# Performance work log

Hardware: AMD Instinct MI355X
Metric: run time of the kernel (lower is better)

## Reference

```python
import jax, jax.numpy as jnp
import numpy as np
import math

B, S, D, H = 2, 2048, 1024, 16
HD = D // H  # head_dim = 64


def setup_inputs() -> dict:
    key = jax.random.key(0)
    k1, k2, k3, k4, k5 = jax.random.split(key, 5)
    scale_in = 1.0 / math.sqrt(D)
    return {
        "x": jax.random.normal(k1, (B, S, D), dtype=jnp.float32),
        "Wqkv": jax.random.normal(k2, (3 * D, D), dtype=jnp.float32) * scale_in,
        "bqkv": jax.random.normal(k3, (3 * D,), dtype=jnp.float32) * 0.01,
        "Wout": jax.random.normal(k4, (D, D), dtype=jnp.float32) * scale_in,
        "bout": jax.random.normal(k5, (D,), dtype=jnp.float32) * 0.01,
    }


def reference(x, Wqkv, bqkv, Wout, bout):
    Bs, Sl, Dm = x.shape
    # qkv projection: torch Linear is x @ W.T + b
    qkv = x @ Wqkv.T + bqkv                        # [B,S,3D]
    qkv = qkv.reshape(Bs, Sl, 3, H, HD)
    q, k, v = qkv[:, :, 0], qkv[:, :, 1], qkv[:, :, 2]  # each [B,S,H,d]
    softmax_scale = 1.0 / math.sqrt(HD)
    # NOTE: source einsum 'bshd,btjd->bsht' sums k over its head axis j.
    # Equivalent efficient form: pre-sum k (and v) over heads.
    k_sum = k.sum(axis=2)                          # [B,S,d]
    v_sum = v.sum(axis=2)                          # [B,S,d]
    scores = jnp.einsum('bshd,btd->bsht', q, k_sum) * softmax_scale  # [B,S,H,T]
    causal_mask = jnp.triu(jnp.ones((Sl, Sl), dtype=bool), k=1)      # [S,T]
    scores = jnp.where(causal_mask[None, :, None, :], -jnp.inf, scores)
    attn = jax.nn.softmax(scores, axis=-1)
    # dropout p=0.0 / eval mode -> identity
    out = jnp.einsum('bsht,btd->bshd', attn, v_sum)  # [B,S,H,d]
    out = out.reshape(Bs, Sl, Dm)
    return out @ Wout.T + bout
```

## Files before the change

### kernel.cpp

```cpp
#include <hip/hip_runtime.h>


#define S_LEN 2048
#define DIM 1024

using floatx4 = __attribute__((ext_vector_type(4))) float;
using halfx8  = __attribute__((ext_vector_type(8))) _Float16;
using halfx4  = __attribute__((ext_vector_type(4))) _Float16;
using halfx2  = __attribute__((ext_vector_type(2))) _Float16;
using fp16x2  = __attribute__((ext_vector_type(2))) __fp16;

__device__ __forceinline__ floatx4 mfma16(halfx8 a, halfx8 b, floatx4 c) {
  return __builtin_amdgcn_mfma_f32_16x16x32_f16(a, b, c, 0, 0, 0);
}

__device__ __forceinline__ void gll16(const void* g, void* l) {
  __builtin_amdgcn_global_load_lds(
      (const __attribute__((address_space(1))) void*)g,
      (__attribute__((address_space(3))) void*)l, 16, 0, 0);
}

__global__ __launch_bounds__(256) void prep_all(
    const float* __restrict__ x, const float* __restrict__ wqkv,
    const float* __restrict__ bqkv, const float* __restrict__ wout,
    _Float16* __restrict__ xb, _Float16* __restrict__ wcomb,
    _Float16* __restrict__ woutb, float* __restrict__ bcomb) {
  int bx = blockIdx.x;
  if (bx < 6144) {
    size_t i4 = ((size_t)bx * 256 + threadIdx.x) * 4;
    const float* src;
    _Float16* dst;
    size_t off;
    if (i4 < 4194304) { src = x; dst = xb; off = i4; }
    else if (i4 < 5242880) { src = wqkv; dst = wcomb; off = i4 - 4194304; }
    else { src = wout; dst = woutb; off = i4 - 5242880; }
    float4 v = *(const float4*)(src + off);
    halfx4 o;
    o[0] = (_Float16)v.x; o[1] = (_Float16)v.y;
    o[2] = (_Float16)v.z; o[3] = (_Float16)v.w;
    *(halfx4*)(dst + off) = o;
  } else {
    int gid = (bx - 6144) * 256 + threadIdx.x;
    int c = gid >> 10, j = gid & 1023;
    int row0 = (c < 64) ? (1024 + c) : (2048 + c - 64);
    float s = 0.f;
#pragma unroll
    for (int h = 0; h < 16; ++h) s += wqkv[(size_t)(row0 + h * 64) * 1024 + j];
    wcomb[(size_t)1024 * 1024 + gid] = (_Float16)s;
    if (gid < 1024) bcomb[gid] = bqkv[gid];
    if (gid < 128) {
      int b0 = (gid < 64) ? (1024 + gid) : (2048 + gid - 64);
      float sb = 0.f;
#pragma unroll
      for (int h = 0; h < 16; ++h) sb += bqkv[b0 + h * 64];
      bcomb[1024 + gid] = sb;
    }
  }
}

template <int MODE>
__global__ __launch_bounds__(256, 6) void gemm_t5(
    const _Float16* __restrict__ A, const _Float16* __restrict__ W,
    const float* __restrict__ bias, void* __restrict__ Cv,
    _Float16* __restrict__ kbo, _Float16* __restrict__ vto) {
  const int K = 1024;
  __shared__ _Float16 As[64][64];
  __shared__ _Float16 Ws[64][64];
  int tid = threadIdx.x;
  int lane = tid & 63, w = tid >> 6, ln = lane & 15, q4 = lane >> 4;
  int m0 = blockIdx.x * 64, n0 = blockIdx.y * 64;
  int rr = lane >> 3, gg = ((lane & 7) ^ rr) * 8;
  const _Float16* agp = A + (size_t)(m0 + w * 16 + rr) * K + gg;
  const _Float16* wgp = W + (size_t)(n0 + w * 16 + rr) * K + gg;
  floatx4 acc[4] = {};
  for (int kt = 0; kt < K; kt += 64) {
    __syncthreads();
    gll16(agp + kt, &As[w * 16][0]);
    gll16(agp + (size_t)8 * K + kt, &As[w * 16 + 8][0]);
    gll16(wgp + kt, &Ws[w * 16][0]);
    gll16(wgp + (size_t)8 * K + kt, &Ws[w * 16 + 8][0]);
    __syncthreads();
#pragma unroll
    for (int kh = 0; kh < 2; ++kh) {
      int sw = ((q4 + 4 * kh) ^ (ln & 7)) * 8;
      halfx8 bf = *(const halfx8*)&Ws[w * 16 + ln][sw];
#pragma unroll
      for (int mf = 0; mf < 4; ++mf) {
        halfx8 af = *(const halfx8*)&As[mf * 16 + ln][sw];
        acc[mf] = mfma16(af, bf, acc[mf]);
      }
    }
  }
  const float qscale = 0.18033688011112042f;
  int col = n0 + w * 16 + ln;
  float bv = bias[col];
  if constexpr (MODE == 1) {
#pragma unroll
    for (int mf = 0; mf < 4; ++mf)
#pragma unroll
      for (int i = 0; i < 4; ++i) {
        int row = m0 + mf * 16 + q4 * 4 + i;
        ((float*)Cv)[(size_t)row * 1024 + col] = acc[mf][i] + bv;
      }
  } else {
    if (col < 1024) {
#pragma unroll
      for (int mf = 0; mf < 4; ++mf)
#pragma unroll
        for (int i = 0; i < 4; ++i) {
          int row = m0 + mf * 16 + q4 * 4 + i;
          ((_Float16*)Cv)[(size_t)row * 1024 + col] =
              (_Float16)((acc[mf][i] + bv) * qscale);
        }
    } else if (col < 1088) {
      int ck = col - 1024;
#pragma unroll
      for (int mf = 0; mf < 4; ++mf)
#pragma unroll
        for (int i = 0; i < 4; ++i) {
          int row = m0 + mf * 16 + q4 * 4 + i;
          kbo[(size_t)row * 64 + ck] = (_Float16)(acc[mf][i] + bv);
        }
    } else {
      int d = col - 1088;
#pragma unroll
      for (int mf = 0; mf < 4; ++mf) {
        int row0 = m0 + mf * 16 + q4 * 4;
        int bb = row0 >> 11, sps = row0 & 2047;
        int blk = sps & ~127, tl = sps & 127;
        int p0 = (tl >> 6) * 64 + ((tl >> 2) & 3) * 8 + ((tl >> 4) & 3) * 2;
        _Float16* basep = &vto[((size_t)((bb << 6) + d)) * S_LEN + blk];
        halfx2 lo, hi;
        lo[0] = (_Float16)(acc[mf][0] + bv);
        lo[1] = (_Float16)(acc[mf][1] + bv);
        hi[0] = (_Float16)(acc[mf][2] + bv);
        hi[1] = (_Float16)(acc[mf][3] + bv);
        *(halfx2*)&basep[p0] = lo;
        *(halfx2*)&basep[p0 + 32] = hi;
      }
    }
  }
}

__global__ __launch_bounds__(512, 4) void flash_attn14(
    const _Float16* __restrict__ Qb, const _Float16* __restrict__ kb,
    const _Float16* __restrict__ vtb, _Float16* __restrict__ aob) {
  __shared__ _Float16 Ks[2][128][64];
  __shared__ _Float16 Vt[2][64][128];
  int tid = threadIdx.x;
  int lane = tid & 63, w = tid >> 6, ln = lane & 15, q4 = lane >> 4;
  int bx = (int)blockIdx.x;
  int lo = bx & 255;
  int b = lo & 1;
  int crow = (bx >> 8) ? (255 - (lo >> 1)) : (lo >> 1);
  int s0 = crow * 8;
  int s = s0 + w;
  size_t bS = (size_t)b * S_LEN;

  int rr = lane >> 3, ggk = ((lane & 7) ^ rr) * 8;
  const _Float16* kgp = kb + (bS + w * 16 + rr) * 64 + ggk;
  int vr = lane >> 4;
  int vhalf = (lane >> 3) & 1, vg = lane & 7;
  const _Float16* vgp[2];
#pragma unroll
  for (int j = 0; j < 2; ++j) {
    int row = w * 8 + 4 * j + vr;
    vgp[j] = vtb + ((size_t)b * 64 + row) * S_LEN + vhalf * 64 +
             ((vg ^ (row & 7)) * 8);
  }
  int swk0 = (q4 ^ (ln & 7)) * 8;
  int swk1 = ((q4 + 4) ^ (ln & 7)) * 8;

  const _Float16* qp = Qb + (bS + s) * DIM + ln * 64 + q4 * 8;
  halfx8 bq0 = *(const halfx8*)qp, bq1 = *(const halfx8*)(qp + 32);

  float m_run = -1e30f, l_run = 0.f;
  floatx4 oacc[4] = {};
  int nt = (crow >> 4) + 1;

  gll16(kgp, &Ks[0][w * 16][0]);
  gll16(kgp + (size_t)8 * 64, &Ks[0][w * 16 + 8][0]);
  gll16(vgp[0], &Vt[0][w * 8][0]);
  gll16(vgp[1], &Vt[0][w * 8 + 4][0]);
  __syncthreads();

  for (int it = 0; it < nt; ++it) {
    int cur = it & 1, nxt = cur ^ 1;
    if (it + 1 < nt) {
      int t1 = (it + 1) << 7;
      gll16(kgp + (size_t)t1 * 64, &Ks[nxt][w * 16][0]);
      gll16(kgp + (size_t)(t1 + 8) * 64, &Ks[nxt][w * 16 + 8][0]);
      gll16(vgp[0] + t1, &Vt[nxt][w * 8][0]);
      gll16(vgp[1] + t1, &Vt[nxt][w * 8 + 4][0]);
    }
    int t0 = it << 7;

    floatx4 sf[2][4];
    __builtin_amdgcn_s_setprio(1);
#pragma unroll
    for (int tq = 0; tq < 2; ++tq)
#pragma unroll
      for (int tf = 0; tf < 4; ++tf) {
        halfx8 ak0 = *(const halfx8*)&Ks[cur][tq * 64 + tf * 16 + ln][swk0];
        halfx8 ak1 = *(const halfx8*)&Ks[cur][tq * 64 + tf * 16 + ln][swk1];
        floatx4 z = {};
        z = mfma16(ak0, bq0, z);
        sf[tq][tf] = mfma16(ak1, bq1, z);
      }
    __builtin_amdgcn_s_setprio(0);
    if (it == nt - 1) {
#pragma unroll
      for (int tq = 0; tq < 2; ++tq)
#pragma unroll
        for (int tf = 0; tf < 4; ++tf)
#pragma unroll
          for (int i = 0; i < 4; ++i) {
            int t = t0 + tq * 64 + tf * 16 + q4 * 4 + i;
            if (t > s) sf[tq][tf][i] = -1e30f;
          }
    }
    float tm = -1e30f;
#pragma unroll
    for (int tq = 0; tq < 2; ++tq)
#pragma unroll
      for (int tf = 0; tf < 4; ++tf)
        tm = fmaxf(tm, fmaxf(fmaxf(sf[tq][tf][0], sf[tq][tf][1]),
                             fmaxf(sf[tq][tf][2], sf[tq][tf][3])));
    tm = fmaxf(tm, __shfl_xor(tm, 16));
    tm = fmaxf(tm, __shfl_xor(tm, 32));
    if (!__all(tm <= m_run + 8.f)) {
      float mn = fmaxf(m_run, tm);
      float alpha = exp2f(m_run - mn);
      m_run = mn;
      l_run *= alpha;
#pragma unroll
      for (int n2 = 0; n2 < 4; ++n2)
#pragma unroll
        for (int i = 0; i < 4; ++i) oacc[n2][i] *= alpha;
    }
    float rs = 0.f;
    unsigned bpw[4][4];
#pragma unroll
    for (int tq = 0; tq < 2; ++tq)
#pragma unroll
      for (int tf = 0; tf < 4; ++tf) {
        float p0 = exp2f(sf[tq][tf][0] - m_run);
        float p1 = exp2f(sf[tq][tf][1] - m_run);
        float p2 = exp2f(sf[tq][tf][2] - m_run);
        float p3 = exp2f(sf[tq][tf][3] - m_run);
        rs += (p0 + p1) + (p2 + p3);
        union { fp16x2 h; unsigned u; } c0, c1;
        c0.h = __builtin_amdgcn_cvt_pkrtz(p0, p1);
        c1.h = __builtin_amdgcn_cvt_pkrtz(p2, p3);
        bpw[2 * tq][tf] = c0.u;
        bpw[2 * tq + 1][tf] = c1.u;
      }
    rs += __shfl_xor(rs, 16);
    rs += __shfl_xor(rs, 32);
    l_run += rs;
    __builtin_amdgcn_s_setprio(1);
#pragma unroll
    for (int kc = 0; kc < 4; ++kc) {
      union { unsigned u[4]; halfx8 v; } bpu;
#pragma unroll
      for (int ww = 0; ww < 4; ++ww) bpu.u[ww] = bpw[kc][ww];
      int half = (kc >> 1) * 64;
      int sw = ((q4 + 4 * (kc & 1)) ^ (ln & 7)) * 8;
#pragma unroll
      for (int n2 = 0; n2 < 4; ++n2) {
        halfx8 av = *(const halfx8*)&Vt[cur][n2 * 16 + ln][half + sw];
        oacc[n2] = mfma16(av, bpu.v, oacc[n2]);
      }
    }
    __builtin_amdgcn_s_setprio(0);
    __syncthreads();
  }
  float inv = 1.0f / l_run;
#pragma unroll
  for (int n2 = 0; n2 < 4; ++n2) {
    halfx4 o;
#pragma unroll
    for (int i = 0; i < 4; ++i) o[i] = (_Float16)(oacc[n2][i] * inv);
    *(halfx4*)(aob + (bS + s) * DIM + ln * 64 + n2 * 16 + q4 * 4) = o;
  }
}

extern "C" void kernel_launch(void* const* d_in, const int* in_sizes, int n_in,
                              void* d_out, int out_size, void* d_ws,
                              size_t ws_size, hipStream_t stream) {
  const float* x    = (const float*)d_in[0];
  const float* wqkv = (const float*)d_in[1];
  const float* bqkv = (const float*)d_in[2];
  const float* wout = (const float*)d_in[3];
  const float* bout = (const float*)d_in[4];
  float* out = (float*)d_out;
  char* ws = (char*)d_ws;
  _Float16* xb    = (_Float16*)(ws);
  _Float16* qb    = (_Float16*)(ws + (8u << 20));
  _Float16* aob   = (_Float16*)(ws + (16u << 20));
  _Float16* kb    = (_Float16*)(ws + (24u << 20));
  _Float16* vtb   = (_Float16*)(ws + (24u << 20) + (512u << 10));
  _Float16* wcomb = (_Float16*)(ws + (25u << 20));
  _Float16* woutb = (_Float16*)(ws + (27u << 20) + (512u << 10));
  float*    bcomb = (float*)(ws + (29u << 20) + (512u << 10));

  hipLaunchKernelGGL(prep_all, dim3(6656), dim3(256), 0, stream,
                     x, wqkv, bqkv, wout, xb, wcomb, woutb, bcomb);
  hipLaunchKernelGGL((gemm_t5<0>), dim3(64, 18), dim3(256), 0, stream,
                     xb, wcomb, bcomb, (void*)qb, kb, vtb);
  hipLaunchKernelGGL(flash_attn14, dim3(512), dim3(512), 0, stream,
                     qb, kb, vtb, aob);
  hipLaunchKernelGGL((gemm_t5<1>), dim3(64, 16), dim3(256), 0, stream,
                     aob, woutb, bout, (void*)out, nullptr, nullptr);
}
```

Baseline: 157.9 us.

## Shrink attention blocks to 4 waves and drop K/V LDS double buffering

Each attention block now has 4 waves covering 4 query rows instead of 8 waves covering 8, and the grid doubles to 1024 blocks, with the causal load-balancing pairing extended to four row groups. K/V tiles are single-buffered in LDS, with a sync before and after each synchronous load in place of prefetching the next tile. This halves LDS per block, allowing more resident blocks and a finer work split. In exchange each wave issues more loads per tile, load latency is no longer overlapped with compute, and total K/V traffic rises because fewer rows share each tile.

```diff
diff --git a/kernel.cpp b/kernel.cpp
--- a/kernel.cpp
+++ b/kernel.cpp
@@ -142,29 +142,30 @@
   }
 }
 
-__global__ __launch_bounds__(512, 4) void flash_attn14(
+__global__ __launch_bounds__(256, 4) void flash_attn15(
     const _Float16* __restrict__ Qb, const _Float16* __restrict__ kb,
     const _Float16* __restrict__ vtb, _Float16* __restrict__ aob) {
-  __shared__ _Float16 Ks[2][128][64];
-  __shared__ _Float16 Vt[2][64][128];
+  __shared__ _Float16 Ks[128][64];
+  __shared__ _Float16 Vt[64][128];
   int tid = threadIdx.x;
   int lane = tid & 63, w = tid >> 6, ln = lane & 15, q4 = lane >> 4;
   int bx = (int)blockIdx.x;
-  int lo = bx & 255;
-  int b = lo & 1;
-  int crow = (bx >> 8) ? (255 - (lo >> 1)) : (lo >> 1);
-  int s0 = crow * 8;
+  int q = bx >> 8, lo = bx & 255;
+  int b = lo & 1, p = lo >> 1;
+  int crow = (q == 0) ? p : (q == 1) ? (255 - p) : (q == 2) ? (256 + p)
+                                                            : (511 - p);
+  int s0 = crow * 4;
   int s = s0 + w;
   size_t bS = (size_t)b * S_LEN;
 
   int rr = lane >> 3, ggk = ((lane & 7) ^ rr) * 8;
-  const _Float16* kgp = kb + (bS + w * 16 + rr) * 64 + ggk;
+  const _Float16* kgp = kb + (bS + w * 32 + rr) * 64 + ggk;
   int vr = lane >> 4;
   int vhalf = (lane >> 3) & 1, vg = lane & 7;
-  const _Float16* vgp[2];
-#pragma unroll
-  for (int j = 0; j < 2; ++j) {
-    int row = w * 8 + 4 * j + vr;
+  const _Float16* vgp[4];
+#pragma unroll
+  for (int j = 0; j < 4; ++j) {
+    int row = w * 16 + 4 * j + vr;
     vgp[j] = vtb + ((size_t)b * 64 + row) * S_LEN + vhalf * 64 +
              ((vg ^ (row & 7)) * 8);
   }
@@ -176,24 +177,18 @@
 
   float m_run = -1e30f, l_run = 0.f;
   floatx4 oacc[4] = {};
-  int nt = (crow >> 4) + 1;
-
-  gll16(kgp, &Ks[0][w * 16][0]);
-  gll16(kgp + (size_t)8 * 64, &Ks[0][w * 16 + 8][0]);
-  gll16(vgp[0], &Vt[0][w * 8][0]);
-  gll16(vgp[1], &Vt[0][w * 8 + 4][0]);
-  __syncthreads();
+  int nt = (crow >> 5) + 1;
 
   for (int it = 0; it < nt; ++it) {
-    int cur = it & 1, nxt = cur ^ 1;
-    if (it + 1 < nt) {
-      int t1 = (it + 1) << 7;
-      gll16(kgp + (size_t)t1 * 64, &Ks[nxt][w * 16][0]);
-      gll16(kgp + (size_t)(t1 + 8) * 64, &Ks[nxt][w * 16 + 8][0]);
-      gll16(vgp[0] + t1, &Vt[nxt][w * 8][0]);
-      gll16(vgp[1] + t1, &Vt[nxt][w * 8 + 4][0]);
-    }
     int t0 = it << 7;
+    __syncthreads();
+#pragma unroll
+    for (int j = 0; j < 4; ++j)
+      gll16(kgp + (size_t)(t0 + 8 * j) * 64, &Ks[w * 32 + 8 * j][0]);
+#pragma unroll
+    for (int j = 0; j < 4; ++j)
+      gll16(vgp[j] + t0, &Vt[w * 16 + 4 * j][0]);
+    __syncthreads();
 
     floatx4 sf[2][4];
     __builtin_amdgcn_s_setprio(1);
@@ -201,8 +196,8 @@
     for (int tq = 0; tq < 2; ++tq)
 #pragma unroll
       for (int tf = 0; tf < 4; ++tf) {
-        halfx8 ak0 = *(const halfx8*)&Ks[cur][tq * 64 + tf * 16 + ln][swk0];
-        halfx8 ak1 = *(const halfx8*)&Ks[cur][tq * 64 + tf * 16 + ln][swk1];
+        halfx8 ak0 = *(const halfx8*)&Ks[tq * 64 + tf * 16 + ln][swk0];
+        halfx8 ak1 = *(const halfx8*)&Ks[tq * 64 + tf * 16 + ln][swk1];
         floatx4 z = {};
         z = mfma16(ak0, bq0, z);
         sf[tq][tf] = mfma16(ak1, bq1, z);
@@ -268,12 +263,11 @@
       int sw = ((q4 + 4 * (kc & 1)) ^ (ln & 7)) * 8;
 #pragma unroll
       for (int n2 = 0; n2 < 4; ++n2) {
-        halfx8 av = *(const halfx8*)&Vt[cur][n2 * 16 + ln][half + sw];
+        halfx8 av = *(const halfx8*)&Vt[n2 * 16 + ln][half + sw];
         oacc[n2] = mfma16(av, bpu.v, oacc[n2]);
       }
     }
     __builtin_amdgcn_s_setprio(0);
-    __syncthreads();
   }
   float inv = 1.0f / l_run;
 #pragma unroll
@@ -308,7 +302,7 @@
                      x, wqkv, bqkv, wout, xb, wcomb, woutb, bcomb);
   hipLaunchKernelGGL((gemm_t5<0>), dim3(64, 18), dim3(256), 0, stream,
                      xb, wcomb, bcomb, (void*)qb, kb, vtb);
-  hipLaunchKernelGGL(flash_attn14, dim3(512), dim3(512), 0, stream,
+  hipLaunchKernelGGL(flash_attn15, dim3(1024), dim3(256), 0, stream,
                      qb, kb, vtb, aob);
   hipLaunchKernelGGL((gemm_t5<1>), dim3(64, 16), dim3(256), 0, stream,
                      aob, woutb, bout, (void*)out, nullptr, nullptr);
```

After: 157.2 us. No clear change (-0.4%).
